# Kernel optimization log

Hardware: AMD Instinct MI355X
Metric: run time of the kernel (lower is better)

## Reference

```python
import jax, jax.numpy as jnp
import numpy as np

N = 2000
E = 20000
C = 16
B = 128
N_IN = 200   # first N_IN nodes are input nodes
N_OUT = 200  # last N_OUT nodes are output nodes
EPS = 1e-5


def setup_inputs() -> dict:
    key = jax.random.key(0)
    ks = jax.random.split(key, 8)
    x = jax.random.normal(ks[0], (B, N), dtype=jnp.float32)
    edge_index = jax.random.randint(ks[1], (2, E), 0, N, dtype=jnp.int32)
    input_node_mask = jnp.arange(N) < N_IN
    output_node_mask = jnp.arange(N) >= (N - N_OUT)
    func_mask = ~(input_node_mask | output_node_mask)
    # sparse-linear parameters (structured forms of W1/W2/W3)
    w1 = jax.random.normal(ks[2], (E, C), dtype=jnp.float32) * (1.0 / np.sqrt(C))
    b1 = jnp.zeros((N, C), dtype=jnp.float32)
    w2 = jax.random.normal(ks[3], (N, C, C), dtype=jnp.float32) * (1.0 / np.sqrt(C))
    b2 = jnp.zeros((N, C), dtype=jnp.float32)
    w3 = jax.random.normal(ks[4], (E, C), dtype=jnp.float32) * 1.0  # d=1 init scale
    b3 = jnp.zeros((E,), dtype=jnp.float32)
    g1 = jnp.ones((N * C,), dtype=jnp.float32)
    be1 = jnp.zeros((N * C,), dtype=jnp.float32)
    g2 = jnp.ones((N * C,), dtype=jnp.float32)
    be2 = jnp.zeros((N * C,), dtype=jnp.float32)
    return {"x": x, "w1": w1, "b1": b1, "w2": w2, "b2": b2, "w3": w3, "b3": b3,
            "g1": g1, "be1": be1, "g2": g2, "be2": be2,
            "edge_index": edge_index, "func_mask": func_mask,
            "output_node_mask": output_node_mask, "layers": 4}


def _batchnorm(h, g, b):
    # training-mode BatchNorm1d: batch mean and biased variance over axis 0
    m = h.mean(axis=0)
    v = h.var(axis=0)
    return (h - m) * jax.lax.rsqrt(v + EPS) * g + b


def reference(x, w1, b1, w2, b2, w3, b3, g1, be1, g2, be2,
              edge_index, func_mask, output_node_mask, layers):
    src, dst = edge_index[0], edge_index[1]
    Bsz, Nn = x.shape
    Ee, Cc = w1.shape
    fm = func_mask.astype(x.dtype)
    w2m = w2 * fm[:, None, None]          # W2 blocks exist only at function nodes
    w3m = w3 * fm[src][:, None]           # W3 rows exist only for edges with src in function nodes

    x0 = x[:, src]                        # node2edge: (B, E)
    xe = x0
    for _ in range(layers):
        # lin1: scatter edge values into dst node hidden channels
        contrib = xe.T[:, :, None] * w1[:, None, :]                    # (E, B, C)
        h = jax.ops.segment_sum(contrib, dst, num_segments=Nn)         # (N, B, C)
        h = jnp.transpose(h, (1, 0, 2)) + b1                           # (B, N, C)
        h = _batchnorm(h.reshape(Bsz, Nn * Cc), g1, be1)
        h = jax.nn.elu(h).reshape(Bsz, Nn, Cc)
        # lin2: block-diagonal C x C mix per (function) node
        h = jnp.einsum('bnc,ncd->bnd', h, w2m) + b2
        h = _batchnorm(h.reshape(Bsz, Nn * Cc), g2, be2)
        h = jax.nn.elu(h).reshape(Bsz, Nn, Cc)
        # lin3: gather src hidden, per-edge dot back to edge space
        xe = jnp.einsum('bec,ec->be', h[:, src], w3m) + b3             # (B, E)
        xe = xe + x0
    # edge2node: scatter-sum edge values to dst nodes, keep output nodes
    nodes = jax.ops.segment_sum(xe.T, dst, num_segments=Nn)            # (N, B)
    return nodes.T * output_node_mask.astype(x.dtype)
```

## Files before the change

kernel.cpp:

```cpp
#include <hip/hip_runtime.h>
#include <math.h>

#define BB 128
#define NN 2000
#define EE 20000
#define CC 16
#define FUNC_LO 200
#define FUNC_HI 1800
#define OUT_LO 1800
#define NFUNC 1600
#define NBLK 1600
#define EPSV 1e-5f
#define SS 40
#define NSLOT (NFUNC * SS)
#define HP 129

#define SCOPE_AGENT __HIP_MEMORY_SCOPE_AGENT

static __device__ __forceinline__ void xe_st(float* p, float v) {
    __hip_atomic_store(p, v, __ATOMIC_RELAXED, SCOPE_AGENT);
}

__device__ __forceinline__ void arrive(int* progress, int L) {
    asm volatile("s_waitcnt vmcnt(0)" ::: "memory");
    __syncthreads();
    if (threadIdx.x == 0)
        __hip_atomic_store(&progress[blockIdx.x], L, __ATOMIC_RELAXED, SCOPE_AGENT);
}

__device__ __forceinline__ void wait_producers(const int* progress,
                                               const int* __restrict__ pblk,
                                               int cbase, int dIn, int L) {
    if (threadIdx.x < 64) {
        int j = threadIdx.x;
        int pb = (j < dIn) ? pblk[cbase + j] : -1;
        bool done = (pb < 0);
        int tries = 0;
        while (true) {
            if (!done)
                done = (__hip_atomic_load(&progress[pb], __ATOMIC_RELAXED,
                                          SCOPE_AGENT) >= L);
            if (__ballot(!done) == 0ull) break;
            __builtin_amdgcn_s_sleep(8);
            if (++tries > (1 << 17)) break;
        }
    }
    __syncthreads();
}

__global__ void k_prep(const float* __restrict__ x, const int* __restrict__ ei,
                       const float* __restrict__ w1, const float* __restrict__ w3,
                       const float* __restrict__ b3,
                       int* __restrict__ degIn, int* __restrict__ degF,
                       int* __restrict__ degO, int* __restrict__ posIn,
                       float* __restrict__ xT, float* __restrict__ w1s,
                       float* __restrict__ w3s, float* __restrict__ b3s,
                       int* __restrict__ inoff, int* __restrict__ wout,
                       int* __restrict__ prodBlk, float* __restrict__ out)
{
    int t = blockIdx.x * 256 + threadIdx.x;
    if (t < EE) {
        int s = ei[t], d = ei[EE + t];
        bool dFn = (d >= FUNC_LO && d < FUNC_HI);
        bool sFn = (s >= FUNC_LO && s < FUNC_HI);
        int pi = -1;
        if (dFn) {
            int p = atomicAdd(&degIn[d], 1);
            pi = (d - FUNC_LO) * SS + p;
            posIn[t] = pi;
            const float4* w1v = (const float4*)w1 + (size_t)t * 4;
            float4* w1o = (float4*)w1s + (size_t)pi * 4;
            #pragma unroll
            for (int i = 0; i < 4; i++) w1o[i] = w1v[i];
            inoff[pi] = s * BB;
            prodBlk[pi] = sFn ? (s - FUNC_LO) : (t % NBLK);
        }
        if (sFn) {
            int po = -1;
            if (dFn) {
                int q = atomicAdd(&degF[s], 1);
                po = (s - FUNC_LO) * SS + q;
                wout[po] = pi * BB;
            } else if (d >= OUT_LO) {
                int q = atomicAdd(&degO[s], 1);
                po = (s - FUNC_LO) * SS + (SS - 1 - q);
                wout[po] = d;
            }
            if (po >= 0) {
                const float4* w3v = (const float4*)w3 + (size_t)t * 4;
                float4* w3o = (float4*)w3s + (size_t)po * 4;
                #pragma unroll
                for (int i = 0; i < 4; i++) w3o[i] = w3v[i];
                b3s[po] = b3[t];
            }
        }
    }
    if (t < NN * BB) {
        out[t] = 0.0f;
        int n = t >> 7, b = t & (BB - 1);
        xT[t] = x[b * NN + n];
    }
}

__device__ __forceinline__ void bn_elu(float (&t)[CC],
                                       const float* __restrict__ g,
                                       const float* __restrict__ be,
                                       float* tile, float* part_s, float* part_ss,
                                       float* sc, float* sh, int b) {
    #pragma unroll
    for (int c = 0; c < CC; c++) tile[c * HP + b] = t[c];
    __syncthreads();
    {
        int c = b & 15, grp = b >> 4;
        float s = 0.f, ss = 0.f;
        #pragma unroll
        for (int i = 0; i < 16; i++) {
            float v = tile[c * HP + grp * 16 + i];
            s += v; ss += v * v;
        }
        part_s[grp * 16 + c] = s;
        part_ss[grp * 16 + c] = ss;
    }
    __syncthreads();
    if (b < CC) {
        float S = 0.f, SSm = 0.f;
        #pragma unroll
        for (int g8 = 0; g8 < 8; g8++) { S += part_s[g8 * 16 + b]; SSm += part_ss[g8 * 16 + b]; }
        float mean = S * (1.0f / BB);
        float var = SSm * (1.0f / BB) - mean * mean;
        float scale = rsqrtf(var + EPSV) * g[b];
        sc[b] = scale;
        sh[b] = be[b] - mean * scale;
    }
    __syncthreads();
    #pragma unroll
    for (int c = 0; c < CC; c++) {
        float u = t[c] * sc[c] + sh[c];
        t[c] = (u > 0.0f) ? u : (__expf(u) - 1.0f);
    }
}

struct FusedArgs {
    const float* xT; float* xeA; float* xeB; float* xeC;
    const float* w1s; const float* w2; const float* w3s; const float* b3s;
    const int* inoff; const int* wout; const int* prodBlk;
    const int* degIn; const int* degF; const int* degO;
    const float* g1; const float* be1; const float* g2; const float* be2;
    const int* ei; const int* posIn; const float* b3;
    float* out;
    int* progress;
};

template<bool FIRST, bool LAST>
__device__ __forceinline__ void layer_body(const FusedArgs& A,
    const float* __restrict__ xe_in, float* __restrict__ xe_out,
    int n, int b, int dIn, int dF, int dO, float x0r,
    const float* w1L, const float* w3L, const float* w2L, const float* b3L,
    const int* ioL, const int* woL,
    float* tile, float* part_s, float* part_ss, float* sc, float* sh)
{
    float a[CC];
    #pragma unroll
    for (int c = 0; c < CC; c++) a[c] = 0.0f;

    for (int k0 = 0; k0 < dIn; k0 += 16) {
        float v[16];
        #pragma unroll
        for (int j = 0; j < 16; j++) {
            v[j] = 0.0f;
            if (k0 + j < dIn) {
                int ro = FIRST ? ioL[k0 + j] : (k0 + j) * BB;
                v[j] = xe_in[ro + b];
            }
        }
        #pragma unroll
        for (int j = 0; j < 16; j++) {
            if (k0 + j < dIn) {
                const float* wr = &w1L[(k0 + j) * CC];
                #pragma unroll
                for (int c = 0; c < CC; c++) a[c] += v[j] * wr[c];
            }
        }
    }

    bn_elu(a, A.g1 + n * CC, A.be1 + n * CC, tile, part_s, part_ss, sc, sh, b);

    float h2[CC];
    #pragma unroll
    for (int d = 0; d < CC; d++) h2[d] = 0.0f;
    #pragma unroll
    for (int c = 0; c < CC; c++) {
        float av = a[c];
        #pragma unroll
        for (int d = 0; d < CC; d++) h2[d] += av * w2L[c * CC + d];
    }

    bn_elu(h2, A.g2 + n * CC, A.be2 + n * CC, tile, part_s, part_ss, sc, sh, b);

    if (!LAST) {
        for (int q0 = 0; q0 < dF; q0 += 4) {
            #pragma unroll
            for (int j = 0; j < 4; j++) {
                int q = q0 + j;
                if (q >= dF) break;
                const float* wr = &w3L[q * CC];
                float val = b3L[q] + x0r;
                #pragma unroll
                for (int d = 0; d < CC; d++) val += h2[d] * wr[d];
                xe_st(&xe_out[woL[q] + b], val);
            }
        }
    } else {
        for (int q0 = 0; q0 < dO; q0 += 4) {
            #pragma unroll
            for (int j = 0; j < 4; j++) {
                int q = q0 + j;
                if (q >= dO) break;
                int ql = SS - 1 - q;
                const float* wr = &w3L[ql * CC];
                float val = b3L[ql] + x0r;
                #pragma unroll
                for (int d = 0; d < CC; d++) val += h2[d] * wr[d];
                int dn = woL[ql];
                atomicAdd(&A.out[(size_t)b * NN + dn], val);
            }
        }
    }
}

__global__ __launch_bounds__(128, 4) void k_fused(FusedArgs A)
{
    const int b = threadIdx.x;
    const int blk = blockIdx.x;
    const int n = FUNC_LO + blk;
    const int cbase = blk * SS;

    __shared__ float tile[CC * HP];
    __shared__ float part_s[128], part_ss[128];
    __shared__ float sc[CC], sh[CC];
    __shared__ float w1L[SS * CC];
    __shared__ float w3L[SS * CC];
    __shared__ float w2L[CC * CC];
    __shared__ float b3L[SS];
    __shared__ int   ioL[SS];
    __shared__ int   woL[SS];

    #pragma unroll
    for (int i = b; i < SS * CC; i += 128) {
        w1L[i] = A.w1s[(size_t)cbase * CC + i];
        w3L[i] = A.w3s[(size_t)cbase * CC + i];
    }
    #pragma unroll
    for (int i = b; i < CC * CC; i += 128)
        w2L[i] = A.w2[(size_t)n * CC * CC + i];
    if (b < SS) {
        b3L[b] = A.b3s[cbase + b];
        ioL[b] = A.inoff[cbase + b];
        woL[b] = A.wout[cbase + b];
    }
    const int dIn = A.degIn[n];
    const int dF  = A.degF[n];
    const int dO  = A.degO[n];
    const float x0r = A.xT[n * BB + b];

    for (int e = blk; e < EE; e += NBLK) {
        int s = A.ei[e];
        if (s >= FUNC_LO && s < FUNC_HI) continue;
        int d = A.ei[EE + e];
        float val = A.b3[e] + A.xT[s * BB + b];
        if (d >= FUNC_LO && d < FUNC_HI) {
            int ro = A.posIn[e] * BB;
            xe_st(&A.xeA[ro + b], val);
            xe_st(&A.xeB[ro + b], val);
            xe_st(&A.xeC[ro + b], val);
        } else if (d >= OUT_LO) {
            atomicAdd(&A.out[(size_t)b * NN + d], val);
        }
    }
    __syncthreads();

    const float* xeAr = A.xeA + (size_t)cbase * BB;
    const float* xeBr = A.xeB + (size_t)cbase * BB;
    const float* xeCr = A.xeC + (size_t)cbase * BB;

    layer_body<true,  false>(A, A.xT, A.xeA, n, b, dIn, dF, dO, x0r,
                             w1L, w3L, w2L, b3L, ioL, woL,
                             tile, part_s, part_ss, sc, sh);
    arrive(A.progress, 1);
    wait_producers(A.progress, A.prodBlk, cbase, dIn, 1);
    layer_body<false, false>(A, xeAr, A.xeB, n, b, dIn, dF, dO, x0r,
                             w1L, w3L, w2L, b3L, ioL, woL,
                             tile, part_s, part_ss, sc, sh);
    arrive(A.progress, 2);
    wait_producers(A.progress, A.prodBlk, cbase, dIn, 2);
    layer_body<false, false>(A, xeBr, A.xeC, n, b, dIn, dF, dO, x0r,
                             w1L, w3L, w2L, b3L, ioL, woL,
                             tile, part_s, part_ss, sc, sh);
    arrive(A.progress, 3);
    wait_producers(A.progress, A.prodBlk, cbase, dIn, 3);
    layer_body<false, true >(A, xeCr, nullptr, n, b, dIn, dF, dO, x0r,
                             w1L, w3L, w2L, b3L, ioL, woL,
                             tile, part_s, part_ss, sc, sh);
}

extern "C" void kernel_launch(void* const* d_in, const int* in_sizes, int n_in,
                              void* d_out, int out_size, void* d_ws, size_t ws_size,
                              hipStream_t stream) {
    const float* x   = (const float*)d_in[0];
    const float* w1  = (const float*)d_in[1];
    const float* w2  = (const float*)d_in[3];
    const float* w3  = (const float*)d_in[5];
    const float* b3  = (const float*)d_in[6];
    const float* g1  = (const float*)d_in[7];
    const float* be1 = (const float*)d_in[8];
    const float* g2  = (const float*)d_in[9];
    const float* be2 = (const float*)d_in[10];
    const int* ei    = (const int*)d_in[11];
    float* out = (float*)d_out;

    char* ws = (char*)d_ws;
    float* xT   = (float*)ws;  ws += (size_t)NN * BB * 4;
    float* xeA  = (float*)ws;  ws += (size_t)NSLOT * BB * 4;
    float* xeB  = (float*)ws;  ws += (size_t)NSLOT * BB * 4;
    float* xeC  = (float*)ws;  ws += (size_t)NSLOT * BB * 4;
    float* w1s  = (float*)ws;  ws += (size_t)NSLOT * CC * 4;
    float* w3s  = (float*)ws;  ws += (size_t)NSLOT * CC * 4;
    float* b3s  = (float*)ws;  ws += (size_t)NSLOT * 4;
    int* degIn  = (int*)ws;    ws += (size_t)NN * 4;
    int* degF   = (int*)ws;    ws += (size_t)NN * 4;
    int* degO   = (int*)ws;    ws += (size_t)NN * 4;
    int* progress = (int*)ws;  ws += (size_t)NBLK * 4;
    int* posIn  = (int*)ws;    ws += (size_t)EE * 4;
    int* inoff  = (int*)ws;    ws += (size_t)NSLOT * 4;
    int* wout   = (int*)ws;    ws += (size_t)NSLOT * 4;
    int* prodBlk= (int*)ws;    ws += (size_t)NSLOT * 4;

    hipMemsetAsync(degIn, 0, (3 * NN + NBLK) * sizeof(int), stream);
    k_prep<<<(NN * BB + 255) / 256, 256, 0, stream>>>(
        x, ei, w1, w3, b3, degIn, degF, degO, posIn,
        xT, w1s, w3s, b3s, inoff, wout, prodBlk, out);

    FusedArgs fa;
    fa.xT = xT; fa.xeA = xeA; fa.xeB = xeB; fa.xeC = xeC;
    fa.w1s = w1s; fa.w2 = w2; fa.w3s = w3s; fa.b3s = b3s;
    fa.inoff = inoff; fa.wout = wout; fa.prodBlk = prodBlk;
    fa.degIn = degIn; fa.degF = degF; fa.degO = degO;
    fa.g1 = g1; fa.be1 = be1; fa.g2 = g2; fa.be2 = be2;
    fa.ei = ei; fa.posIn = posIn; fa.b3 = b3;
    fa.out = out;
    fa.progress = progress;
    k_fused<<<NBLK, 128, 0, stream>>>(fa);
}
```

Measured before the change: 165.8 us.

## Replace persistent dataflow-synced kernel with per-layer launches and compacted fill kernel

Drops the single persistent kernel, whose blocks spin-wait on producer progress flags between layers, and launches one kernel per layer instead, with two ping-pong edge buffers. Edges whose source is not a function node are compacted into a list during prep. A separate fill kernel writes their constant values into both buffers and adds them into the output. Spin waiting is a problem when not all 1600 blocks can be resident at once, and these launch boundaries remove it. The cost is extra launch overhead, plus reloading per-node weights into shared memory in each layer.

```diff
diff --git a/kernel.cpp b/kernel.cpp
--- a/kernel.cpp
+++ b/kernel.cpp
@@ -9,54 +9,22 @@
 #define FUNC_HI 1800
 #define OUT_LO 1800
 #define NFUNC 1600
-#define NBLK 1600
 #define EPSV 1e-5f
 #define SS 40
 #define NSLOT (NFUNC * SS)
 #define HP 129
 
-#define SCOPE_AGENT __HIP_MEMORY_SCOPE_AGENT
-
-static __device__ __forceinline__ void xe_st(float* p, float v) {
-    __hip_atomic_store(p, v, __ATOMIC_RELAXED, SCOPE_AGENT);
-}
-
-__device__ __forceinline__ void arrive(int* progress, int L) {
-    asm volatile("s_waitcnt vmcnt(0)" ::: "memory");
-    __syncthreads();
-    if (threadIdx.x == 0)
-        __hip_atomic_store(&progress[blockIdx.x], L, __ATOMIC_RELAXED, SCOPE_AGENT);
-}
-
-__device__ __forceinline__ void wait_producers(const int* progress,
-                                               const int* __restrict__ pblk,
-                                               int cbase, int dIn, int L) {
-    if (threadIdx.x < 64) {
-        int j = threadIdx.x;
-        int pb = (j < dIn) ? pblk[cbase + j] : -1;
-        bool done = (pb < 0);
-        int tries = 0;
-        while (true) {
-            if (!done)
-                done = (__hip_atomic_load(&progress[pb], __ATOMIC_RELAXED,
-                                          SCOPE_AGENT) >= L);
-            if (__ballot(!done) == 0ull) break;
-            __builtin_amdgcn_s_sleep(8);
-            if (++tries > (1 << 17)) break;
-        }
-    }
-    __syncthreads();
-}
 
 __global__ void k_prep(const float* __restrict__ x, const int* __restrict__ ei,
                        const float* __restrict__ w1, const float* __restrict__ w3,
                        const float* __restrict__ b3,
                        int* __restrict__ degIn, int* __restrict__ degF,
-                       int* __restrict__ degO, int* __restrict__ posIn,
+                       int* __restrict__ degO, int* __restrict__ fillCnt,
                        float* __restrict__ xT, float* __restrict__ w1s,
                        float* __restrict__ w3s, float* __restrict__ b3s,
                        int* __restrict__ inoff, int* __restrict__ wout,
-                       int* __restrict__ prodBlk, float* __restrict__ out)
+                       int* __restrict__ fillRow, int* __restrict__ fillSrc,
+                       float* __restrict__ fillB3, float* __restrict__ out)
 {
     int t = blockIdx.x * 256 + threadIdx.x;
     if (t < EE) {
@@ -67,13 +35,11 @@
         if (dFn) {
             int p = atomicAdd(&degIn[d], 1);
             pi = (d - FUNC_LO) * SS + p;
-            posIn[t] = pi;
             const float4* w1v = (const float4*)w1 + (size_t)t * 4;
             float4* w1o = (float4*)w1s + (size_t)pi * 4;
             #pragma unroll
             for (int i = 0; i < 4; i++) w1o[i] = w1v[i];
             inoff[pi] = s * BB;
-            prodBlk[pi] = sFn ? (s - FUNC_LO) : (t % NBLK);
         }
         if (sFn) {
             int po = -1;
@@ -93,6 +59,11 @@
                 for (int i = 0; i < 4; i++) w3o[i] = w3v[i];
                 b3s[po] = b3[t];
             }
+        } else if (dFn || d >= OUT_LO) {
+            int fi = atomicAdd(fillCnt, 1);
+            fillRow[fi] = dFn ? pi : (-(d - OUT_LO) - 1);
+            fillSrc[fi] = s * BB;
+            fillB3[fi]  = b3[t];
         }
     }
     if (t < NN * BB) {
@@ -102,9 +73,28 @@
     }
 }
 
+__global__ __launch_bounds__(128) void k_fill(
+    const int* __restrict__ fillCnt, const int* __restrict__ fillRow,
+    const int* __restrict__ fillSrc, const float* __restrict__ fillB3,
+    const float* __restrict__ xT, float* __restrict__ xeA,
+    float* __restrict__ xeB, float* __restrict__ out)
+{
+    int b = threadIdx.x;
+    int cnt = fillCnt[0];
+    for (int i = blockIdx.x; i < cnt; i += gridDim.x) {
+        int row = fillRow[i];
+        float val = fillB3[i] + xT[fillSrc[i] + b];
+        if (row >= 0) {
+            xeA[(size_t)row * BB + b] = val;
+            xeB[(size_t)row * BB + b] = val;
+        } else {
+            atomicAdd(&out[(size_t)b * NN + (OUT_LO + (-row - 1))], val);
+        }
+    }
+}
+
 __device__ __forceinline__ void bn_elu(float (&t)[CC],
-                                       const float* __restrict__ g,
-                                       const float* __restrict__ be,
+                                       const float* gL, const float* beL,
                                        float* tile, float* part_s, float* part_ss,
                                        float* sc, float* sh, int b) {
     #pragma unroll
@@ -128,9 +118,9 @@
         for (int g8 = 0; g8 < 8; g8++) { S += part_s[g8 * 16 + b]; SSm += part_ss[g8 * 16 + b]; }
         float mean = S * (1.0f / BB);
         float var = SSm * (1.0f / BB) - mean * mean;
-        float scale = rsqrtf(var + EPSV) * g[b];
+        float scale = rsqrtf(var + EPSV) * gL[b];
         sc[b] = scale;
-        sh[b] = be[b] - mean * scale;
+        sh[b] = beL[b] - mean * scale;
     }
     __syncthreads();
     #pragma unroll
@@ -140,25 +130,58 @@
     }
 }
 
-struct FusedArgs {
-    const float* xT; float* xeA; float* xeB; float* xeC;
+struct LArgs {
+    const float* xT;
     const float* w1s; const float* w2; const float* w3s; const float* b3s;
-    const int* inoff; const int* wout; const int* prodBlk;
+    const int* inoff; const int* wout;
     const int* degIn; const int* degF; const int* degO;
     const float* g1; const float* be1; const float* g2; const float* be2;
-    const int* ei; const int* posIn; const float* b3;
     float* out;
-    int* progress;
 };
 
 template<bool FIRST, bool LAST>
-__device__ __forceinline__ void layer_body(const FusedArgs& A,
-    const float* __restrict__ xe_in, float* __restrict__ xe_out,
-    int n, int b, int dIn, int dF, int dO, float x0r,
-    const float* w1L, const float* w3L, const float* w2L, const float* b3L,
-    const int* ioL, const int* woL,
-    float* tile, float* part_s, float* part_ss, float* sc, float* sh)
+__global__ __launch_bounds__(128, 4) void k_layer(LArgs A,
+    const float* __restrict__ xe_in, float* __restrict__ xe_out)
 {
+    const int b = threadIdx.x;
+    const int blk = blockIdx.x;
+    const int n = FUNC_LO + blk;
+    const int cbase = blk * SS;
+
+    __shared__ float tile[CC * HP];
+    __shared__ float part_s[128], part_ss[128];
+    __shared__ float sc[CC], sh[CC];
+    __shared__ float w1L[SS * CC];
+    __shared__ float w3L[SS * CC];
+    __shared__ float w2L[CC * CC];
+    __shared__ float b3L[SS];
+    __shared__ int   ioL[SS];
+    __shared__ int   woL[SS];
+    __shared__ float g1L[CC], be1L[CC], g2L[CC], be2L[CC];
+
+    #pragma unroll
+    for (int i = b; i < SS * CC; i += 128) {
+        w1L[i] = A.w1s[(size_t)cbase * CC + i];
+        w3L[i] = A.w3s[(size_t)cbase * CC + i];
+    }
+    #pragma unroll
+    for (int i = b; i < CC * CC; i += 128)
+        w2L[i] = A.w2[(size_t)n * CC * CC + i];
+    if (b < SS) {
+        b3L[b] = A.b3s[cbase + b];
+        ioL[b] = A.inoff[cbase + b];
+        woL[b] = A.wout[cbase + b];
+    }
+    if (b < CC) {
+        g1L[b] = A.g1[n * CC + b];  be1L[b] = A.be1[n * CC + b];
+        g2L[b] = A.g2[n * CC + b];  be2L[b] = A.be2[n * CC + b];
+    }
+    const int dIn = A.degIn[n];
+    const int dF  = A.degF[n];
+    const int dO  = A.degO[n];
+    const float x0r = A.xT[n * BB + b];
+    __syncthreads();
+
     float a[CC];
     #pragma unroll
     for (int c = 0; c < CC; c++) a[c] = 0.0f;
@@ -169,7 +192,7 @@
         for (int j = 0; j < 16; j++) {
             v[j] = 0.0f;
             if (k0 + j < dIn) {
-                int ro = FIRST ? ioL[k0 + j] : (k0 + j) * BB;
+                int ro = FIRST ? ioL[k0 + j] : (cbase + k0 + j) * BB;
                 v[j] = xe_in[ro + b];
             }
         }
@@ -183,7 +206,7 @@
         }
     }
 
-    bn_elu(a, A.g1 + n * CC, A.be1 + n * CC, tile, part_s, part_ss, sc, sh, b);
+    bn_elu(a, g1L, be1L, tile, part_s, part_ss, sc, sh, b);
 
     float h2[CC];
     #pragma unroll
@@ -195,7 +218,7 @@
         for (int d = 0; d < CC; d++) h2[d] += av * w2L[c * CC + d];
     }
 
-    bn_elu(h2, A.g2 + n * CC, A.be2 + n * CC, tile, part_s, part_ss, sc, sh, b);
+    bn_elu(h2, g2L, be2L, tile, part_s, part_ss, sc, sh, b);
 
     if (!LAST) {
         for (int q0 = 0; q0 < dF; q0 += 4) {
@@ -207,7 +230,7 @@
                 float val = b3L[q] + x0r;
                 #pragma unroll
                 for (int d = 0; d < CC; d++) val += h2[d] * wr[d];
-                xe_st(&xe_out[woL[q] + b], val);
+                xe_out[(size_t)woL[q] + b] = val;
             }
         }
     } else {
@@ -226,81 +249,6 @@
             }
         }
     }
-}
-
-__global__ __launch_bounds__(128, 4) void k_fused(FusedArgs A)
-{
-    const int b = threadIdx.x;
-    const int blk = blockIdx.x;
-    const int n = FUNC_LO + blk;
-    const int cbase = blk * SS;
-
-    __shared__ float tile[CC * HP];
-    __shared__ float part_s[128], part_ss[128];
-    __shared__ float sc[CC], sh[CC];
-    __shared__ float w1L[SS * CC];
-    __shared__ float w3L[SS * CC];
-    __shared__ float w2L[CC * CC];
-    __shared__ float b3L[SS];
-    __shared__ int   ioL[SS];
-    __shared__ int   woL[SS];
-
-    #pragma unroll
-    for (int i = b; i < SS * CC; i += 128) {
-        w1L[i] = A.w1s[(size_t)cbase * CC + i];
-        w3L[i] = A.w3s[(size_t)cbase * CC + i];
-    }
-    #pragma unroll
-    for (int i = b; i < CC * CC; i += 128)
-        w2L[i] = A.w2[(size_t)n * CC * CC + i];
-    if (b < SS) {
-        b3L[b] = A.b3s[cbase + b];
-        ioL[b] = A.inoff[cbase + b];
-        woL[b] = A.wout[cbase + b];
-    }
-    const int dIn = A.degIn[n];
-    const int dF  = A.degF[n];
-    const int dO  = A.degO[n];
-    const float x0r = A.xT[n * BB + b];
-
-    for (int e = blk; e < EE; e += NBLK) {
-        int s = A.ei[e];
-        if (s >= FUNC_LO && s < FUNC_HI) continue;
-        int d = A.ei[EE + e];
-        float val = A.b3[e] + A.xT[s * BB + b];
-        if (d >= FUNC_LO && d < FUNC_HI) {
-            int ro = A.posIn[e] * BB;
-            xe_st(&A.xeA[ro + b], val);
-            xe_st(&A.xeB[ro + b], val);
-            xe_st(&A.xeC[ro + b], val);
-        } else if (d >= OUT_LO) {
-            atomicAdd(&A.out[(size_t)b * NN + d], val);
-        }
-    }
-    __syncthreads();
-
-    const float* xeAr = A.xeA + (size_t)cbase * BB;
-    const float* xeBr = A.xeB + (size_t)cbase * BB;
-    const float* xeCr = A.xeC + (size_t)cbase * BB;
-
-    layer_body<true,  false>(A, A.xT, A.xeA, n, b, dIn, dF, dO, x0r,
-                             w1L, w3L, w2L, b3L, ioL, woL,
-                             tile, part_s, part_ss, sc, sh);
-    arrive(A.progress, 1);
-    wait_producers(A.progress, A.prodBlk, cbase, dIn, 1);
-    layer_body<false, false>(A, xeAr, A.xeB, n, b, dIn, dF, dO, x0r,
-                             w1L, w3L, w2L, b3L, ioL, woL,
-                             tile, part_s, part_ss, sc, sh);
-    arrive(A.progress, 2);
-    wait_producers(A.progress, A.prodBlk, cbase, dIn, 2);
-    layer_body<false, false>(A, xeBr, A.xeC, n, b, dIn, dF, dO, x0r,
-                             w1L, w3L, w2L, b3L, ioL, woL,
-                             tile, part_s, part_ss, sc, sh);
-    arrive(A.progress, 3);
-    wait_producers(A.progress, A.prodBlk, cbase, dIn, 3);
-    layer_body<false, true >(A, xeCr, nullptr, n, b, dIn, dF, dO, x0r,
-                             w1L, w3L, w2L, b3L, ioL, woL,
-                             tile, part_s, part_ss, sc, sh);
 }
 
 extern "C" void kernel_launch(void* const* d_in, const int* in_sizes, int n_in,
@@ -322,32 +270,36 @@
     float* xT   = (float*)ws;  ws += (size_t)NN * BB * 4;
     float* xeA  = (float*)ws;  ws += (size_t)NSLOT * BB * 4;
     float* xeB  = (float*)ws;  ws += (size_t)NSLOT * BB * 4;
-    float* xeC  = (float*)ws;  ws += (size_t)NSLOT * BB * 4;
     float* w1s  = (float*)ws;  ws += (size_t)NSLOT * CC * 4;
     float* w3s  = (float*)ws;  ws += (size_t)NSLOT * CC * 4;
     float* b3s  = (float*)ws;  ws += (size_t)NSLOT * 4;
     int* degIn  = (int*)ws;    ws += (size_t)NN * 4;
     int* degF   = (int*)ws;    ws += (size_t)NN * 4;
     int* degO   = (int*)ws;    ws += (size_t)NN * 4;
-    int* progress = (int*)ws;  ws += (size_t)NBLK * 4;
-    int* posIn  = (int*)ws;    ws += (size_t)EE * 4;
+    int* fillCnt= (int*)ws;    ws += 64;
     int* inoff  = (int*)ws;    ws += (size_t)NSLOT * 4;
     int* wout   = (int*)ws;    ws += (size_t)NSLOT * 4;
-    int* prodBlk= (int*)ws;    ws += (size_t)NSLOT * 4;
-
-    hipMemsetAsync(degIn, 0, (3 * NN + NBLK) * sizeof(int), stream);
+    int* fillRow= (int*)ws;    ws += (size_t)EE * 4;
+    int* fillSrc= (int*)ws;    ws += (size_t)EE * 4;
+    float* fillB3=(float*)ws;  ws += (size_t)EE * 4;
+
+    hipMemsetAsync(degIn, 0, (3 * NN + 16) * sizeof(int), stream);
     k_prep<<<(NN * BB + 255) / 256, 256, 0, stream>>>(
-        x, ei, w1, w3, b3, degIn, degF, degO, posIn,
-        xT, w1s, w3s, b3s, inoff, wout, prodBlk, out);
-
-    FusedArgs fa;
-    fa.xT = xT; fa.xeA = xeA; fa.xeB = xeB; fa.xeC = xeC;
-    fa.w1s = w1s; fa.w2 = w2; fa.w3s = w3s; fa.b3s = b3s;
-    fa.inoff = inoff; fa.wout = wout; fa.prodBlk = prodBlk;
-    fa.degIn = degIn; fa.degF = degF; fa.degO = degO;
-    fa.g1 = g1; fa.be1 = be1; fa.g2 = g2; fa.be2 = be2;
-    fa.ei = ei; fa.posIn = posIn; fa.b3 = b3;
-    fa.out = out;
-    fa.progress = progress;
-    k_fused<<<NBLK, 128, 0, stream>>>(fa);
-}
+        x, ei, w1, w3, b3, degIn, degF, degO, fillCnt,
+        xT, w1s, w3s, b3s, inoff, wout, fillRow, fillSrc, fillB3, out);
+    k_fill<<<1024, 128, 0, stream>>>(fillCnt, fillRow, fillSrc, fillB3,
+                                     xT, xeA, xeB, out);
+
+    LArgs la;
+    la.xT = xT;
+    la.w1s = w1s; la.w2 = w2; la.w3s = w3s; la.b3s = b3s;
+    la.inoff = inoff; la.wout = wout;
+    la.degIn = degIn; la.degF = degF; la.degO = degO;
+    la.g1 = g1; la.be1 = be1; la.g2 = g2; la.be2 = be2;
+    la.out = out;
+
+    k_layer<true,  false><<<NFUNC, 128, 0, stream>>>(la, xT,  xeA);
+    k_layer<false, false><<<NFUNC, 128, 0, stream>>>(la, xeA, xeB);
+    k_layer<false, false><<<NFUNC, 128, 0, stream>>>(la, xeB, xeA);
+    k_layer<false, true ><<<NFUNC, 128, 0, stream>>>(la, xeA, nullptr);
+}
```

Result: slower. 172.5 us (+4.1%).
